# Kernel tuning notes

Hardware: AMD Instinct MI355X
Metric: run time of the kernel (lower is better)

## Reference

```python
import jax, jax.numpy as jnp
import numpy as np

B, S, HID = 2, 2048, 4096
NH, NKV, HD = 32, 8, 128
GROUPS = NH // NKV
THETA = 10000.0
SUPPRESS = 0.1


def setup_inputs() -> dict:
    key = jax.random.key(0)
    ks = jax.random.split(key, 8)
    hidden_states = jax.random.normal(ks[0], (B, S, HID), jnp.float32)
    sc = 0.02
    Wq = jax.random.normal(ks[1], (NH * HD, HID), jnp.float32) * sc
    Wk = jax.random.normal(ks[2], (NKV * HD, HID), jnp.float32) * sc
    Wv = jax.random.normal(ks[3], (NKV * HD, HID), jnp.float32) * sc
    Wo = jax.random.normal(ks[4], (HID, NH * HD), jnp.float32) * sc
    # additive causal mask [B,1,S,S]
    causal = jnp.where(jnp.tril(jnp.ones((S, S), bool)), 0.0, jnp.finfo(jnp.float32).min)
    attention_mask = jnp.broadcast_to(causal[None, None], (B, 1, S, S)).astype(jnp.float32)
    position_ids = jnp.broadcast_to(jnp.arange(S, dtype=jnp.int32)[None], (B, S))
    tgt_pos = jax.random.randint(ks[5], (B,), S // 2, S, dtype=jnp.int32)
    subject_positions = jax.random.randint(ks[6], (B, 8), 0, S // 2, dtype=jnp.int32)
    return dict(hidden_states=hidden_states, Wq=Wq, Wk=Wk, Wv=Wv, Wo=Wo,
                attention_mask=attention_mask, position_ids=position_ids,
                tgt_pos=tgt_pos, subject_positions=subject_positions)


def _rope_cos_sin(position_ids):
    inv_freq = 1.0 / (THETA ** (jnp.arange(0, HD, 2, dtype=jnp.float32) / HD))  # [HD/2]
    freqs = position_ids.astype(jnp.float32)[:, :, None] * inv_freq[None, None, :]  # [B,S,HD/2]
    emb = jnp.concatenate([freqs, freqs], axis=-1)  # [B,S,HD]
    return jnp.cos(emb), jnp.sin(emb)


def _rotate_half(x):
    x1, x2 = jnp.split(x, 2, axis=-1)
    return jnp.concatenate([-x2, x1], axis=-1)


def reference(hidden_states, Wq, Wk, Wv, Wo, attention_mask, position_ids, tgt_pos, subject_positions):
    b, s, _ = hidden_states.shape
    q = (hidden_states @ Wq.T).reshape(b, s, NH, HD).transpose(0, 2, 1, 3)   # [B,NH,S,HD]
    k = (hidden_states @ Wk.T).reshape(b, s, NKV, HD).transpose(0, 2, 1, 3)  # [B,NKV,S,HD]
    v = (hidden_states @ Wv.T).reshape(b, s, NKV, HD).transpose(0, 2, 1, 3)

    cos, sin = _rope_cos_sin(position_ids)  # [B,S,HD]
    cos, sin = cos[:, None], sin[:, None]   # broadcast over heads
    q = q * cos + _rotate_half(q) * sin
    k = k * cos + _rotate_half(k) * sin

    # repeat_kv for GQA
    k = jnp.repeat(k, GROUPS, axis=1)  # [B,NH,S,HD]
    v = jnp.repeat(v, GROUPS, axis=1)

    attn = jnp.einsum('bhqd,bhkd->bhqk', q, k) / jnp.sqrt(jnp.float32(HD))
    attn = attn + attention_mask
    attn = jax.nn.softmax(attn.astype(jnp.float32), axis=-1).astype(q.dtype)

    # per-token suppression: attn[b,:,tgt_pos[b],subject_positions[b,:]] *= c
    b_idx = jnp.arange(b)
    attn = attn.at[b_idx[:, None], :, tgt_pos[:, None], subject_positions].multiply(SUPPRESS)

    out = jnp.einsum('bhqk,bhkd->bhqd', attn, v)        # [B,NH,S,HD]
    out = out.transpose(0, 2, 1, 3).reshape(b, s, NH * HD)
    return out @ Wo.T
```

## Files before the change

kernel.cpp:

```cpp
#include <hip/hip_runtime.h>
#include <math.h>

typedef float f32x4 __attribute__((ext_vector_type(4)));
typedef unsigned int u32x4 __attribute__((ext_vector_type(4)));
typedef unsigned short u16x4 __attribute__((ext_vector_type(4)));
typedef __bf16 bf16x8 __attribute__((ext_vector_type(8)));

#define SCALE_Q 0.08838834764831845f

__device__ __forceinline__ float bf2f(unsigned short u) {
  unsigned int x = ((unsigned int)u) << 16;
  return __builtin_bit_cast(float, x);
}
__device__ __forceinline__ unsigned short f2bf(float f) {
  unsigned int u = __builtin_bit_cast(unsigned int, f);
  u += 0x7fffu + ((u >> 16) & 1u);
  return (unsigned short)(u >> 16);
}

__device__ __forceinline__ void gload_lds16(const unsigned short* g, unsigned short* l) {
  __builtin_amdgcn_global_load_lds((const __attribute__((address_space(1))) unsigned int*)g,
                                   (__attribute__((address_space(3))) unsigned int*)l,
                                   16, 0, 0);
}

__global__ __launch_bounds__(256) void cvt_bf16(const float* __restrict__ in,
                                                unsigned short* __restrict__ out, int n4) {
  int i = blockIdx.x * 256 + threadIdx.x;
  if (i >= n4) return;
  f32x4 v = *(const f32x4*)(in + (size_t)i * 4);
  u16x4 o;
  o[0] = f2bf(v[0]); o[1] = f2bf(v[1]); o[2] = f2bf(v[2]); o[3] = f2bf(v[3]);
  *(u16x4*)(out + (size_t)i * 4) = o;
}

template <int BF16OUT>
__global__ __launch_bounds__(512, 2) void gemm256(const unsigned short* __restrict__ A,
                                                  const unsigned short* __restrict__ B,
                                                  float* __restrict__ Cf,
                                                  unsigned short* __restrict__ Cb,
                                                  int M, int N, int K) {
  extern __shared__ __align__(16) unsigned short lds[];
  const int tid = threadIdx.x, lane = tid & 63, wv = tid >> 6;
  const int l16 = lane & 15, g16 = lane >> 4;
  const int m0 = blockIdx.y * 256, n0 = blockIdx.x * 256;
  const int wm = (wv >> 2) * 128, wn = (wv & 3) * 64;

  const unsigned short* aptr[4];
  const unsigned short* bptr[4];
  int adst[4], bdst[4];
#pragma unroll
  for (int j = 0; j < 4; ++j) {
    int S = (wv < 4) ? (4 * j + wv) : (16 + 4 * j + (wv - 4));
    int row = (S >> 1) * 16 + (lane >> 2);
    int col = (S & 1) * 32 + (((lane & 3) * 8) ^ ((lane >> 5) << 4));
    aptr[j] = A + (size_t)(m0 + row) * K + col;
    bptr[j] = B + (size_t)(n0 + row) * K + col;
    adst[j] = S * 512;
    bdst[j] = 16384 + S * 512;
  }

#define SLOT(j, bufoff, koff)                              \
  do {                                                     \
    gload_lds16(aptr[j] + (koff), lds + (bufoff) + adst[j]); \
    gload_lds16(bptr[j] + (koff), lds + (bufoff) + bdst[j]); \
  } while (0)

  f32x4 acc[8][4] = {};
  const int NT = K >> 6;

  SLOT(0, 0, 0); SLOT(1, 0, 0); SLOT(2, 0, 0); SLOT(3, 0, 0);
  SLOT(0, 32768, 64); SLOT(1, 32768, 64); SLOT(2, 32768, 64);
  asm volatile("s_waitcnt vmcnt(6)" ::: "memory");
  __builtin_amdgcn_s_barrier();

  const int rdo = l16 * 32 + ((g16 * 8) ^ ((l16 >> 3) << 4));

  for (int t = 0; t < NT; ++t) {
    const int p = t & 1;
    const unsigned short* La = lds + p * 32768;
    const unsigned short* Lb = La + 16384;
    const int cur = p * 32768, oth = 32768 - cur;
    const int kn1 = ((t + 1 < NT) ? t + 1 : NT - 1) * 64;
    const int kn2 = ((t + 2 < NT) ? t + 2 : NT - 1) * 64;

    bf16x8 bfr[4][2];

    {
#pragma unroll
      for (int ni = 0; ni < 4; ++ni) {
        int sb = ((wn + ni * 16) >> 4) * 2;
#pragma unroll
        for (int ks = 0; ks < 2; ++ks)
          bfr[ni][ks] = *(const bf16x8*)&Lb[(sb + ks) * 512 + rdo];
      }
      bf16x8 afr[2][2];
#pragma unroll
      for (int j = 0; j < 2; ++j) {
        int sb = ((wm + j * 16) >> 4) * 2;
#pragma unroll
        for (int ks = 0; ks < 2; ++ks)
          afr[j][ks] = *(const bf16x8*)&La[(sb + ks) * 512 + rdo];
      }
      SLOT(3, oth, kn1);
      __builtin_amdgcn_s_barrier();
      asm volatile("s_waitcnt lgkmcnt(0)" ::: "memory");
      __builtin_amdgcn_sched_barrier(0);
      __builtin_amdgcn_s_setprio(1);
#pragma unroll
      for (int j = 0; j < 2; ++j)
#pragma unroll
        for (int ni = 0; ni < 4; ++ni)
#pragma unroll
          for (int ks = 0; ks < 2; ++ks)
            acc[j][ni] = __builtin_amdgcn_mfma_f32_16x16x32_bf16(
                afr[j][ks], bfr[ni][ks], acc[j][ni], 0, 0, 0);
      __builtin_amdgcn_s_setprio(0);
      __builtin_amdgcn_s_barrier();
    }

#pragma unroll
    for (int q = 1; q < 4; ++q) {
      bf16x8 afr[2][2];
#pragma unroll
      for (int j = 0; j < 2; ++j) {
        int sb = ((wm + (q * 2 + j) * 16) >> 4) * 2;
#pragma unroll
        for (int ks = 0; ks < 2; ++ks)
          afr[j][ks] = *(const bf16x8*)&La[(sb + ks) * 512 + rdo];
      }
      if (q == 1) SLOT(0, cur, kn2);
      if (q == 2) SLOT(1, cur, kn2);
      if (q == 3) {
        SLOT(2, cur, kn2);
        asm volatile("s_waitcnt vmcnt(6)" ::: "memory");
      }
      __builtin_amdgcn_s_barrier();
      asm volatile("s_waitcnt lgkmcnt(0)" ::: "memory");
      __builtin_amdgcn_sched_barrier(0);
      __builtin_amdgcn_s_setprio(1);
#pragma unroll
      for (int j = 0; j < 2; ++j)
#pragma unroll
        for (int ni = 0; ni < 4; ++ni)
#pragma unroll
          for (int ks = 0; ks < 2; ++ks)
            acc[q * 2 + j][ni] = __builtin_amdgcn_mfma_f32_16x16x32_bf16(
                afr[j][ks], bfr[ni][ks], acc[q * 2 + j][ni], 0, 0, 0);
      __builtin_amdgcn_s_setprio(0);
      __builtin_amdgcn_s_barrier();
    }
  }
  asm volatile("s_waitcnt vmcnt(0)" ::: "memory");
#undef SLOT

#pragma unroll
  for (int mi = 0; mi < 8; ++mi)
#pragma unroll
    for (int ni = 0; ni < 4; ++ni) {
      int row = m0 + wm + mi * 16 + g16 * 4;
      int col = n0 + wn + ni * 16 + l16;
#pragma unroll
      for (int r = 0; r < 4; ++r) {
        if (BF16OUT) Cb[(size_t)(row + r) * N + col] = f2bf(acc[mi][ni][r]);
        else         Cf[(size_t)(row + r) * N + col] = acc[mi][ni][r];
      }
    }
}

__global__ __launch_bounds__(256) void rope_cvt(const unsigned short* __restrict__ C1,
                                                const int* __restrict__ pos_ids,
                                                unsigned short* __restrict__ Qb,
                                                unsigned short* __restrict__ Kb) {
  int idx = blockIdx.x * 256 + threadIdx.x;
  int i = idx & 63;
  int t = idx >> 6;
  int head = t % 40;
  int m = t / 40;
  int b = m >> 11, s = m & 2047;
  const unsigned short* src = C1 + (size_t)m * 6144 + head * 128;
  float x1 = bf2f(src[i]), x2 = bf2f(src[i + 64]);
  float invf = exp2f((float)i * -0.2076205059304601f);
  float ang = (float)pos_ids[m] * invf;
  float c, sn;
  sincosf(ang, &sn, &c);
  float o1 = x1 * c - x2 * sn;
  float o2 = x2 * c + x1 * sn;
  unsigned short* dst;
  float scl = 1.0f;
  if (head < 32) {
    dst = Qb + ((size_t)(b * 32 + head) * 2048 + s) * 128;
    scl = SCALE_Q;
  } else {
    dst = Kb + ((size_t)(b * 8 + head - 32) * 2048 + s) * 128;
  }
  dst[i] = f2bf(o1 * scl);
  dst[i + 64] = f2bf(o2 * scl);
}

__global__ __launch_bounds__(256) void vtrans(const unsigned short* __restrict__ C1,
                                              unsigned short* __restrict__ Vt) {
  __shared__ __align__(16) unsigned short T[64 * 72];
  const int s0 = blockIdx.x * 64, d0 = blockIdx.y * 64, bh = blockIdx.z;
  const int t = threadIdx.x;
  {
    int sl = t >> 2, c16 = (t & 3) * 16;
    const unsigned short* src =
        C1 + (size_t)((bh >> 3) * 2048 + s0 + sl) * 6144 + 5120 + (bh & 7) * 128 + d0 + c16;
    u32x4 a0 = *(const u32x4*)src;
    u32x4 a1 = *(const u32x4*)(src + 8);
    *(u32x4*)&T[sl * 72 + c16] = a0;
    *(u32x4*)&T[sl * 72 + c16 + 8] = a1;
  }
  __syncthreads();
  {
    int dl = t >> 2, s16 = (t & 3) * 16;
    unsigned short* dst = Vt + ((size_t)bh * 128 + d0 + dl) * 2048 + s0 + s16;
    u16x4 o[4];
#pragma unroll
    for (int j = 0; j < 16; ++j) ((unsigned short*)o)[j] = T[(s16 + j) * 72 + dl];
#pragma unroll
    for (int q = 0; q < 4; ++q) *(u16x4*)(dst + q * 4) = o[q];
  }
}

__global__ __launch_bounds__(512, 4) void flash_fwd(const unsigned short* __restrict__ Q,
                                                    const unsigned short* __restrict__ K,
                                                    const unsigned short* __restrict__ Vt,
                                                    unsigned short* __restrict__ AO) {
  __shared__ __align__(16) unsigned short Ks[64 * 128];
  __shared__ __align__(16) unsigned short VT[128 * 64];
  __shared__ __align__(16) unsigned short Pl[128 * 72];

  const int id = blockIdx.x;
  const int xs = id & 7;
  const int kk = id >> 3;
  const int s = xs + 8 * (kk >> 5);
  const int bis = kk & 31;
  const int b = s >> 3, kvh = s & 7;
  const int h = kvh * 4 + (bis >> 3);
  const int qpair = bis & 7;

  const int tid = threadIdx.x, lane = tid & 63, wv = tid >> 6;
  const int l16 = lane & 15, g16 = lane >> 4;
  const unsigned short* Qp = Q + (size_t)(b * 32 + h) * 2048 * 128;
  const unsigned short* Kp = K + (size_t)(b * 8 + kvh) * 2048 * 128;
  const unsigned short* Vp = Vt + (size_t)(b * 8 + kvh) * 128 * 2048;

  const int st_row = tid >> 4;
  const int st_cb = (tid & 15) * 16;
  const int vd = tid >> 2;
  const int vq = (tid & 3) * 32;

  char* ksdst[2];
  char* vtdst[2];
#pragma unroll
  for (int p = 0; p < 2; ++p)
    ksdst[p] = (char*)Ks + (p * 32 + st_row) * 256 + (st_cb ^ ((st_row & 7) << 4));
#pragma unroll
  for (int e = 0; e < 2; ++e)
    vtdst[e] = (char*)VT + vd * 128 + ((vq + e * 16) ^ ((vd & 7) << 4));

  for (int pass = 0; pass < 2; ++pass) {
    const int qt = pass == 0 ? (15 - qpair) : qpair;
    const int nkb = 2 * qt + 2;

    bf16x8 qf[4];
    {
      int qrow = qt * 128 + wv * 16 + l16;
#pragma unroll
      for (int ks = 0; ks < 4; ++ks)
        qf[ks] = *(const bf16x8*)&Qp[(size_t)qrow * 128 + ks * 32 + g16 * 8];
    }

    float m_r[4] = {-1e30f, -1e30f, -1e30f, -1e30f};
    float l_r[4] = {0.f, 0.f, 0.f, 0.f};
    f32x4 ao[8] = {};

    u32x4 kreg[2], vreg[2];
#pragma unroll
    for (int p = 0; p < 2; ++p)
      kreg[p] = *(const u32x4*)&Kp[(size_t)(p * 32 + st_row) * 128 + (st_cb >> 1)];
#pragma unroll
    for (int e = 0; e < 2; ++e)
      vreg[e] = *(const u32x4*)&Vp[(size_t)vd * 2048 + (vq >> 1) + e * 8];

    for (int kb = 0; kb < nkb; ++kb) {
      __syncthreads();
#pragma unroll
      for (int p = 0; p < 2; ++p) *(u32x4*)ksdst[p] = kreg[p];
#pragma unroll
      for (int e = 0; e < 2; ++e) *(u32x4*)vtdst[e] = vreg[e];
      if (kb + 1 < nkb) {
#pragma unroll
        for (int p = 0; p < 2; ++p)
          kreg[p] = *(const u32x4*)&Kp[(size_t)((kb + 1) * 64 + p * 32 + st_row) * 128 +
                                       (st_cb >> 1)];
#pragma unroll
        for (int e = 0; e < 2; ++e)
          vreg[e] = *(const u32x4*)&Vp[(size_t)vd * 2048 + (kb + 1) * 64 + (vq >> 1) + e * 8];
      }
      __syncthreads();

      f32x4 sc[4] = {};
      __builtin_amdgcn_s_setprio(1);
#pragma unroll
      for (int kt = 0; kt < 4; ++kt) {
#pragma unroll
        for (int ks = 0; ks < 4; ++ks) {
          int row = kt * 16 + l16;
          int cb = ks * 64 + g16 * 16;
          bf16x8 kf = *(const bf16x8*)((const char*)Ks + row * 256 + (cb ^ ((row & 7) << 4)));
          sc[kt] = __builtin_amdgcn_mfma_f32_16x16x32_bf16(qf[ks], kf, sc[kt], 0, 0, 0);
        }
      }
      __builtin_amdgcn_s_setprio(0);

      int qrow0 = qt * 128 + wv * 16 + g16 * 4;
      float p_[4][4];
      if (kb >= 2 * qt) {
#pragma unroll
        for (int kt = 0; kt < 4; ++kt)
#pragma unroll
          for (int r = 0; r < 4; ++r) {
            int kc = kb * 64 + kt * 16 + l16;
            p_[kt][r] = (kc <= qrow0 + r) ? sc[kt][r] : -INFINITY;
          }
      } else {
#pragma unroll
        for (int kt = 0; kt < 4; ++kt)
#pragma unroll
          for (int r = 0; r < 4; ++r) p_[kt][r] = sc[kt][r];
      }

      float rescv[4];
      bool anyresc = false;
#pragma unroll
      for (int r = 0; r < 4; ++r) {
        float mx = fmaxf(fmaxf(p_[0][r], p_[1][r]), fmaxf(p_[2][r], p_[3][r]));
#pragma unroll
        for (int off = 8; off; off >>= 1) mx = fmaxf(mx, __shfl_xor(mx, off));
        float mnew = fmaxf(m_r[r], mx);
        bool keep = (mnew - m_r[r]) <= 8.0f;
        float mu = keep ? m_r[r] : mnew;
        rescv[r] = keep ? 1.0f : __expf(m_r[r] - mnew);
        anyresc |= !keep;
        m_r[r] = mu;
        float rsum = 0.f;
#pragma unroll
        for (int kt = 0; kt < 4; ++kt) {
          float e = __expf(p_[kt][r] - mu);
          p_[kt][r] = e;
          rsum += e;
        }
#pragma unroll
        for (int off = 8; off; off >>= 1) rsum += __shfl_xor(rsum, off);
        l_r[r] = l_r[r] * rescv[r] + rsum;
      }
      if (__any(anyresc ? 1 : 0)) {
#pragma unroll
        for (int dt = 0; dt < 8; ++dt)
#pragma unroll
          for (int r = 0; r < 4; ++r) ao[dt][r] *= rescv[r];
      }

#pragma unroll
      for (int kt = 0; kt < 4; ++kt)
#pragma unroll
        for (int r = 0; r < 4; ++r)
          Pl[(wv * 16 + g16 * 4 + r) * 72 + kt * 16 + l16] = f2bf(p_[kt][r]);

      bf16x8 pa[2];
#pragma unroll
      for (int kc = 0; kc < 2; ++kc)
        pa[kc] = *(const bf16x8*)&Pl[(wv * 16 + l16) * 72 + kc * 32 + g16 * 8];

      __builtin_amdgcn_s_setprio(1);
#pragma unroll
      for (int dt = 0; dt < 8; ++dt) {
#pragma unroll
        for (int kc = 0; kc < 2; ++kc) {
          bf16x8 vf = *(const bf16x8*)((const char*)VT + (dt * 16 + l16) * 128 +
                                       ((kc * 64 + g16 * 16) ^ ((l16 & 7) << 4)));
          ao[dt] = __builtin_amdgcn_mfma_f32_16x16x32_bf16(pa[kc], vf, ao[dt], 0, 0, 0);
        }
      }
      __builtin_amdgcn_s_setprio(0);
    }

    int qrow = qt * 128 + wv * 16 + g16 * 4;
#pragma unroll
    for (int r = 0; r < 4; ++r) {
      float inv = 1.0f / l_r[r];
#pragma unroll
      for (int dt = 0; dt < 8; ++dt)
        AO[((size_t)b * 2048 + qrow + r) * 4096 + h * 128 + dt * 16 + l16] =
            f2bf(ao[dt][r] * inv);
    }
  }
}

__global__ __launch_bounds__(256) void suppress_fix(const unsigned short* __restrict__ Q,
                                                    const unsigned short* __restrict__ K,
                                                    const unsigned short* __restrict__ Vt,
                                                    const int* __restrict__ tgt,
                                                    const int* __restrict__ subj,
                                                    unsigned short* __restrict__ AO) {
  const int h = blockIdx.x, b = blockIdx.y;
  const int tid = threadIdx.x, lane = tid & 63, wv = tid >> 6;
  __shared__ float qv[128];
  __shared__ float warr[2048];
  __shared__ float sred[4];
  int row = tgt[b];
  const unsigned short* Qp = Q + ((size_t)(b * 32 + h) * 2048 + row) * 128;
  const unsigned short* Kp = K + (size_t)(b * 8 + (h >> 2)) * 2048 * 128;
  const unsigned short* Vp = Vt + (size_t)(b * 8 + (h >> 2)) * 128 * 2048;
  if (tid < 128) qv[tid] = bf2f(Qp[tid]);
  __syncthreads();
  int nk = row + 1;
  float lmax = -1e30f;
  for (int j = tid; j < nk; j += 256) {
    const unsigned short* kr = Kp + (size_t)j * 128;
    float s = 0.f;
    for (int d = 0; d < 128; d += 8) {
      u32x4 kv = *(const u32x4*)&kr[d];
      const unsigned short* kk = (const unsigned short*)&kv;
#pragma unroll
      for (int e = 0; e < 8; ++e) s += qv[d + e] * bf2f(kk[e]);
    }
    warr[j] = s;
    lmax = fmaxf(lmax, s);
  }
#pragma unroll
  for (int off = 32; off; off >>= 1) lmax = fmaxf(lmax, __shfl_xor(lmax, off));
  if (lane == 0) sred[wv] = lmax;
  __syncthreads();
  float mx = fmaxf(fmaxf(sred[0], sred[1]), fmaxf(sred[2], sred[3]));
  __syncthreads();
  float lsum = 0.f;
  for (int j = tid; j < nk; j += 256) {
    float w = __expf(warr[j] - mx);
    lsum += w;
    float f = 1.f;
#pragma unroll
    for (int i2 = 0; i2 < 8; ++i2)
      if (subj[b * 8 + i2] == j) f *= 0.1f;
    warr[j] = w * f;
  }
#pragma unroll
  for (int off = 32; off; off >>= 1) lsum += __shfl_xor(lsum, off);
  if (lane == 0) sred[wv] = lsum;
  __syncthreads();
  float tot = sred[0] + sred[1] + sred[2] + sred[3];
  if (tid < 128) {
    float acc = 0.f;
    const unsigned short* vr = Vp + (size_t)tid * 2048;
    int nk8 = nk & ~7;
    for (int j0 = 0; j0 < nk8; j0 += 8) {
      u32x4 vv = *(const u32x4*)&vr[j0];
      const unsigned short* v8 = (const unsigned short*)&vv;
#pragma unroll
      for (int e = 0; e < 8; ++e) acc += warr[j0 + e] * bf2f(v8[e]);
    }
    for (int j = nk8; j < nk; ++j) acc += warr[j] * bf2f(vr[j]);
    AO[((size_t)b * 2048 + row) * 4096 + h * 128 + tid] = f2bf(acc / tot);
  }
}

extern "C" void kernel_launch(void* const* d_in, const int* in_sizes, int n_in,
                              void* d_out, int out_size, void* d_ws, size_t ws_size,
                              hipStream_t stream) {
  const float* hidden = (const float*)d_in[0];
  const float* Wq = (const float*)d_in[1];
  const float* Wk = (const float*)d_in[2];
  const float* Wv = (const float*)d_in[3];
  const float* Wo = (const float*)d_in[4];
  const int* pos = (const int*)d_in[6];
  const int* tgt = (const int*)d_in[7];
  const int* subj = (const int*)d_in[8];
  float* out = (float*)d_out;

  unsigned short* ws = (unsigned short*)d_ws;
  unsigned short* Xb    = ws;
  unsigned short* Wqkvb = Xb + (size_t)16777216;
  unsigned short* Wob   = Wqkvb + (size_t)25165824;
  unsigned short* C1    = Wob + (size_t)16777216;
  unsigned short* Qb    = C1 + (size_t)25165824;
  unsigned short* Kb    = Qb + (size_t)16777216;
  unsigned short* Vt    = Kb + (size_t)4194304;
  unsigned short* AO    = Vt + (size_t)4194304;

  (void)hipFuncSetAttribute(reinterpret_cast<const void*>(gemm256<1>),
                            hipFuncAttributeMaxDynamicSharedMemorySize, 131072);
  (void)hipFuncSetAttribute(reinterpret_cast<const void*>(gemm256<0>),
                            hipFuncAttributeMaxDynamicSharedMemorySize, 131072);

  cvt_bf16<<<16384, 256, 0, stream>>>(hidden, Xb, 4194304);
  cvt_bf16<<<16384, 256, 0, stream>>>(Wq, Wqkvb, 4194304);
  cvt_bf16<<<4096, 256, 0, stream>>>(Wk, Wqkvb + (size_t)16777216, 1048576);
  cvt_bf16<<<4096, 256, 0, stream>>>(Wv, Wqkvb + (size_t)20971520, 1048576);
  cvt_bf16<<<16384, 256, 0, stream>>>(Wo, Wob, 4194304);

  gemm256<1><<<dim3(24, 16), 512, 131072, stream>>>(Xb, Wqkvb, nullptr, C1, 4096, 6144, 4096);

  rope_cvt<<<40960, 256, 0, stream>>>(C1, pos, Qb, Kb);

  vtrans<<<dim3(32, 2, 16), 256, 0, stream>>>(C1, Vt);

  flash_fwd<<<512, 512, 0, stream>>>(Qb, Kb, Vt, AO);

  suppress_fix<<<dim3(32, 2), 256, 0, stream>>>(Qb, Kb, Vt, tgt, subj, AO);

  gemm256<0><<<dim3(16, 16), 512, 131072, stream>>>(AO, Wob, out, nullptr, 4096, 4096, 4096);
}
```

Before: 645.7 us.

## Add BK=32 double-buffered QKV GEMM kernel with split-phase prefetch

```diff
diff --git a/kernel.cpp b/kernel.cpp
--- a/kernel.cpp
+++ b/kernel.cpp
@@ -32,6 +32,112 @@
   u16x4 o;
   o[0] = f2bf(v[0]); o[1] = f2bf(v[1]); o[2] = f2bf(v[2]); o[3] = f2bf(v[3]);
   *(u16x4*)(out + (size_t)i * 4) = o;
+}
+
+__global__ __launch_bounds__(512, 4) void gemm256_bk32(const unsigned short* __restrict__ A,
+                                                       const unsigned short* __restrict__ B,
+                                                       unsigned short* __restrict__ Cb,
+                                                       int M, int N, int K) {
+  extern __shared__ __align__(16) unsigned short lds[];
+  const int tid = threadIdx.x, lane = tid & 63, wv = tid >> 6;
+  const int l16 = lane & 15, g16 = lane >> 4;
+  const int m0 = blockIdx.y * 256, n0 = blockIdx.x * 256;
+  const int wm = (wv >> 2) * 128, wn = (wv & 3) * 64;
+
+  const int srow = lane >> 2;
+  const int scol = ((lane & 3) * 8) ^ ((lane >> 5) << 4);
+  const int S_A0 = (wv < 4) ? wv : wv + 4;
+  const int S_A1 = (wv < 4) ? wv + 4 : wv + 8;
+  const unsigned short* aRA = A + (size_t)(m0 + S_A0 * 16 + srow) * K + scol;
+  const unsigned short* aRB = A + (size_t)(m0 + S_A1 * 16 + srow) * K + scol;
+  const unsigned short* bB0 = B + (size_t)(n0 + wv * 16 + srow) * K + scol;
+  const unsigned short* bB1 = B + (size_t)(n0 + (8 + wv) * 16 + srow) * K + scol;
+  const int dRA = S_A0 * 512, dRB = S_A1 * 512;
+  const int dB0 = 8192 + wv * 512, dB1 = 8192 + (8 + wv) * 512;
+
+  f32x4 acc[8][4] = {};
+  const int NT = K >> 5;
+
+  gload_lds16(aRA, lds + dRA);
+  gload_lds16(bB0, lds + dB0);
+  gload_lds16(aRB, lds + dRB);
+  gload_lds16(bB1, lds + dB1);
+  gload_lds16(aRA + 32, lds + 16384 + dRA);
+  gload_lds16(bB0 + 32, lds + 16384 + dB0);
+  asm volatile("s_waitcnt vmcnt(2)" ::: "memory");
+  __builtin_amdgcn_s_barrier();
+
+  const int rdo = l16 * 32 + ((g16 * 8) ^ ((l16 >> 3) << 4));
+  const int SaBase = wm >> 4;
+  const int SbBase = (wn >> 4);
+
+  for (int t = 0; t < NT; ++t) {
+    const int cur = (t & 1) * 16384, oth = 16384 - cur;
+    const unsigned short* La = lds + cur;
+    const unsigned short* Lb = La + 8192;
+    const int kn1 = ((t + 1 < NT) ? t + 1 : NT - 1) * 32;
+    const int kn2 = ((t + 2 < NT) ? t + 2 : NT - 1) * 32;
+
+    bf16x8 bfr[4];
+
+    {
+#pragma unroll
+      for (int ni = 0; ni < 4; ++ni)
+        bfr[ni] = *(const bf16x8*)&Lb[(SbBase + ni) * 512 + rdo];
+      bf16x8 afr[4];
+#pragma unroll
+      for (int j = 0; j < 4; ++j)
+        afr[j] = *(const bf16x8*)&La[(SaBase + j) * 512 + rdo];
+      gload_lds16(aRB + kn1, lds + oth + dRB);
+      gload_lds16(bB1 + kn1, lds + oth + dB1);
+      __builtin_amdgcn_s_barrier();
+      asm volatile("s_waitcnt lgkmcnt(0)" ::: "memory");
+      __builtin_amdgcn_sched_barrier(0);
+      __builtin_amdgcn_s_setprio(1);
+#pragma unroll
+      for (int j = 0; j < 4; ++j)
+#pragma unroll
+        for (int ni = 0; ni < 4; ++ni)
+          acc[j][ni] = __builtin_amdgcn_mfma_f32_16x16x32_bf16(
+              afr[j], bfr[ni], acc[j][ni], 0, 0, 0);
+      __builtin_amdgcn_s_setprio(0);
+      __builtin_amdgcn_s_barrier();
+    }
+
+    {
+      bf16x8 afr[4];
+#pragma unroll
+      for (int j = 0; j < 4; ++j)
+        afr[j] = *(const bf16x8*)&La[(SaBase + 4 + j) * 512 + rdo];
+      gload_lds16(aRA + kn2, lds + cur + dRA);
+      gload_lds16(bB0 + kn2, lds + cur + dB0);
+      asm volatile("s_waitcnt vmcnt(2)" ::: "memory");
+      __builtin_amdgcn_s_barrier();
+      asm volatile("s_waitcnt lgkmcnt(0)" ::: "memory");
+      __builtin_amdgcn_sched_barrier(0);
+      __builtin_amdgcn_s_setprio(1);
+#pragma unroll
+      for (int j = 0; j < 4; ++j)
+#pragma unroll
+        for (int ni = 0; ni < 4; ++ni)
+          acc[4 + j][ni] = __builtin_amdgcn_mfma_f32_16x16x32_bf16(
+              afr[j], bfr[ni], acc[4 + j][ni], 0, 0, 0);
+      __builtin_amdgcn_s_setprio(0);
+      __builtin_amdgcn_s_barrier();
+    }
+  }
+  asm volatile("s_waitcnt vmcnt(0)" ::: "memory");
+
+#pragma unroll
+  for (int mi = 0; mi < 8; ++mi)
+#pragma unroll
+    for (int ni = 0; ni < 4; ++ni) {
+      int row = m0 + wm + mi * 16 + g16 * 4;
+      int col = n0 + wn + ni * 16 + l16;
+#pragma unroll
+      for (int r = 0; r < 4; ++r)
+        Cb[(size_t)(row + r) * N + col] = f2bf(acc[mi][ni][r]);
+    }
 }
 
 template <int BF16OUT>
@@ -490,8 +596,8 @@
   unsigned short* Vt    = Kb + (size_t)4194304;
   unsigned short* AO    = Vt + (size_t)4194304;
 
-  (void)hipFuncSetAttribute(reinterpret_cast<const void*>(gemm256<1>),
-                            hipFuncAttributeMaxDynamicSharedMemorySize, 131072);
+  (void)hipFuncSetAttribute(reinterpret_cast<const void*>(gemm256_bk32),
+                            hipFuncAttributeMaxDynamicSharedMemorySize, 65536);
   (void)hipFuncSetAttribute(reinterpret_cast<const void*>(gemm256<0>),
                             hipFuncAttributeMaxDynamicSharedMemorySize, 131072);
 
@@ -501,7 +607,7 @@
   cvt_bf16<<<4096, 256, 0, stream>>>(Wv, Wqkvb + (size_t)20971520, 1048576);
   cvt_bf16<<<16384, 256, 0, stream>>>(Wo, Wob, 4194304);
 
-  gemm256<1><<<dim3(24, 16), 512, 131072, stream>>>(Xb, Wqkvb, nullptr, C1, 4096, 6144, 4096);
+  gemm256_bk32<<<dim3(24, 16), 512, 65536, stream>>>(Xb, Wqkvb, C1, 4096, 6144, 4096);
 
   rope_cvt<<<40960, 256, 0, stream>>>(C1, pos, Qb, Kb);
 
```

New measurement: 2.087 ms. +223.2%, slower.
